# Performance work log

Measured on AMD Instinct MI355X. Metric: run time of the kernel, lower is better.

The kernel has to match this reference:

```python
import jax, jax.numpy as jnp
import numpy as np

N = 4_194_304
B = 64
H = 16
TAU = 1.0


def setup_inputs() -> dict:
    key = jax.random.key(0)
    ks = jax.random.split(key, 8)
    pos = jax.random.normal(ks[0], (N, 3), dtype=jnp.float32)
    reflectance = jax.random.uniform(ks[1], (N,), dtype=jnp.float32)
    batch = jnp.sort(jax.random.randint(ks[2], (N,), 0, B).astype(jnp.int32))
    gumbels = jax.random.gumbel(ks[3], (B, 2), dtype=jnp.float32)
    W1 = jax.random.normal(ks[4], (4, H), dtype=jnp.float32) * 0.5
    b1 = jnp.zeros((H,), dtype=jnp.float32)
    W2 = jax.random.normal(ks[5], (H, H), dtype=jnp.float32) * 0.25
    b2 = jnp.zeros((H,), dtype=jnp.float32)
    Wg = jax.random.normal(ks[6], (H, 2), dtype=jnp.float32) * 0.25
    bg = jnp.array([0.0, 2.0], dtype=jnp.float32)  # gate_nn bias init per module
    return {"pos": pos, "reflectance": reflectance, "batch": batch, "gumbels": gumbels,
            "W1": W1, "b1": b1, "W2": W2, "b2": b2, "Wg": Wg, "bg": bg}


def reference(pos, reflectance, batch, gumbels, W1, b1, W2, b2, Wg, bg):
    # point-wise MLP: [N,4] -> [N,H]
    features = jnp.concatenate([pos, reflectance[:, None]], axis=-1)
    h = jax.nn.relu(features @ W1 + b1)
    h = jax.nn.relu(h @ W2 + b2)
    # batch-indexed max pool: [N,H] -> [B,H]
    sample_features = jax.ops.segment_max(h, batch, num_segments=B)
    gate_logits = sample_features @ Wg + bg  # [B,2]
    # gumbel-softmax (hard=False as in forward)
    gate_decision = jax.nn.softmax((gate_logits + gumbels) / TAU, axis=-1)
    # gather per-point gate and scale reflectance
    use_reflectance = gate_decision[:, 1][batch]  # [N]
    return use_reflectance * reflectance
```

## Files before the change

kernel.cpp:

```cpp
#include <hip/hip_runtime.h>
#include <hip/hip_bf16.h>


#define N_PTS 4194304
#define NB 64
#define NH 16
#define WPB 4
#define SITERS 4
#define PTW (256 * SITERS)
#define PPB (WPB * PTW)
#define NBLK (N_PTS / PPB)
#define NENT (NBLK * 2)

typedef __attribute__((ext_vector_type(8))) short bf16x8;
typedef __attribute__((ext_vector_type(4))) float f32x4;
union U8 { bf16x8 v; unsigned u[4]; unsigned short s[8]; };

struct Rec { int idA, idB, bpos; };

__device__ __forceinline__ unsigned pk2(float a, float b) {
    float2 t; t.x = a; t.y = b;
    __hip_bfloat162 r = __float22bfloat162_rn(t);
    unsigned u;
    __builtin_memcpy(&u, &r, sizeof(u));
    return u;
}
__device__ __forceinline__ unsigned short f2bf(float x) {
    unsigned u = __float_as_uint(x);
    u = u + 0x7fffu + ((u >> 16) & 1u);
    return (unsigned short)(u >> 16);
}

template<bool SLOW>
__device__ __forceinline__ void do_chunk(
    const float4& q0, const float4& q1, const float4& q2, const float4& rr,
    int sb, int g, int col, int bposw,
    const U8& A1, const U8& A2, const f32x4& c1, const f32x4& c2,
    f32x4& accA, f32x4& accB)
{
    const float f[4][4] = {{q0.x, q0.y, q0.z, rr.x},
                           {q0.w, q1.x, q1.y, rr.y},
                           {q1.z, q1.w, q2.x, rr.z},
                           {q2.y, q2.z, q2.w, rr.w}};
#pragma unroll
    for (int j = 0; j < 4; ++j) {
        const unsigned F01 = pk2(f[j][0], f[j][1]);
        const unsigned F23 = pk2(f[j][2], f[j][3]);
        f32x4 d[4], h[4];
#pragma unroll
        for (int t = 0; t < 4; ++t) {
            const bool mine = (g == t);
            U8 B;
            B.u[0] = mine ? F01 : 0u;
            B.u[1] = mine ? F23 : 0u;
            B.u[2] = 0u; B.u[3] = 0u;
            d[t] = __builtin_amdgcn_mfma_f32_16x16x32_bf16(A1.v, B.v, c1, 0, 0, 0);
        }
#pragma unroll
        for (int t = 0; t < 4; ++t) {
            U8 P;
            P.u[0] = pk2(fmaxf(d[t][0], 0.f), fmaxf(d[t][1], 0.f));
            P.u[1] = pk2(fmaxf(d[t][2], 0.f), fmaxf(d[t][3], 0.f));
            P.u[2] = 0u; P.u[3] = 0u;
            h[t] = __builtin_amdgcn_mfma_f32_16x16x32_bf16(A2.v, P.v, c2, 0, 0, 0);
        }
#pragma unroll
        for (int t = 0; t < 4; ++t) {
            if (!SLOW) {
#pragma unroll
                for (int r = 0; r < 4; ++r) accA[r] = fmaxf(accA[r], h[t][r]);
            } else {
                const bool m = (sb + 4 * (16 * t + col) + j) < bposw;
#pragma unroll
                for (int r = 0; r < 4; ++r) {
                    accA[r] = fmaxf(accA[r], m ? h[t][r] : 0.f);
                    accB[r] = fmaxf(accB[r], m ? 0.f : h[t][r]);
                }
            }
        }
    }
}

__global__ __launch_bounds__(256, 4) void mlp_segmax_kernel(
    const float* __restrict__ pos,
    const float* __restrict__ refl,
    const int*   __restrict__ batch,
    const float* __restrict__ W1, const float* __restrict__ b1,
    const float* __restrict__ W2, const float* __restrict__ b2,
    float* __restrict__ pv,
    int*   __restrict__ pid,
    Rec*   __restrict__ recs)
{
    __shared__ float wlds[352];
    __shared__ float lv[WPB][2][NH];
    __shared__ int   li[WPB][2];
    __shared__ int   lbp[WPB];

    const int tid  = threadIdx.x;
    const int lane = tid & 63;
    const int wid  = tid >> 6;
    const int col  = lane & 15;
    const int g    = lane >> 4;
    const int wb   = (blockIdx.x * WPB + wid) * PTW;

    if (tid < 64)  wlds[tid]        = W1[tid];
    if (tid < 16)  wlds[64 + tid]   = b1[tid];
    wlds[80 + tid] = W2[tid];
    if (tid < 16)  wlds[336 + tid]  = b2[tid];
    __syncthreads();

    U8 A1, A2;
#pragma unroll
    for (int e = 0; e < 4; ++e) {
        A1.s[e]     = f2bf(wlds[e * NH + col]);
        A1.s[e + 4] = 0;
        A2.s[e]     = f2bf(wlds[80 + (4 * g + e) * NH + col]);
        A2.s[e + 4] = 0;
    }
    f32x4 c1, c2;
#pragma unroll
    for (int r = 0; r < 4; ++r) {
        c1[r] = wlds[64 + 4 * g + r];
        c2[r] = wlds[336 + 4 * g + r];
    }

    const int idA = batch[wb];
    const int idB = batch[wb + PTW - 1];
    const bool isSlow = (idA != idB);

    f32x4 accA = {0.f, 0.f, 0.f, 0.f};
    f32x4 accB = {0.f, 0.f, 0.f, 0.f};

    const float4* gp = (const float4*)(pos + (size_t)wb * 3);
    const float4* gr = (const float4*)(refl + wb);

    float4 q0 = gp[3 * lane + 0];
    float4 q1 = gp[3 * lane + 1];
    float4 q2 = gp[3 * lane + 2];
    float4 rr = gr[lane];

    if (!isSlow) {
#pragma unroll
        for (int s = 0; s < SITERS; ++s) {
            float4 n0, n1, n2, nr;
            if (s + 1 < SITERS) {
                n0 = gp[(s + 1) * 192 + 3 * lane + 0];
                n1 = gp[(s + 1) * 192 + 3 * lane + 1];
                n2 = gp[(s + 1) * 192 + 3 * lane + 2];
                nr = gr[(s + 1) * 64 + lane];
            }
            do_chunk<false>(q0, q1, q2, rr, wb + s * 256, g, col, 0,
                            A1, A2, c1, c2, accA, accB);
            if (s + 1 < SITERS) { q0 = n0; q1 = n1; q2 = n2; rr = nr; }
        }
    } else {
        int bposw = 0x7fffffff;
        for (int it = 0; it < PTW / 64; ++it) {
            const int idx = wb + it * 64 + lane;
            const unsigned long long mk = __ballot(batch[idx] != idA);
            if (mk) bposw = min(bposw, wb + it * 64 + (__ffsll((long long)mk) - 1));
        }
#pragma unroll
        for (int s = 0; s < SITERS; ++s) {
            float4 n0, n1, n2, nr;
            if (s + 1 < SITERS) {
                n0 = gp[(s + 1) * 192 + 3 * lane + 0];
                n1 = gp[(s + 1) * 192 + 3 * lane + 1];
                n2 = gp[(s + 1) * 192 + 3 * lane + 2];
                nr = gr[(s + 1) * 64 + lane];
            }
            do_chunk<true>(q0, q1, q2, rr, wb + s * 256, g, col, bposw,
                           A1, A2, c1, c2, accA, accB);
            if (s + 1 < SITERS) { q0 = n0; q1 = n1; q2 = n2; rr = nr; }
        }
        lbp[wid] = bposw;
    }

#pragma unroll
    for (int mk = 1; mk <= 8; mk <<= 1) {
#pragma unroll
        for (int r = 0; r < 4; ++r) {
            accA[r] = fmaxf(accA[r], __shfl_xor(accA[r], mk));
            accB[r] = fmaxf(accB[r], __shfl_xor(accB[r], mk));
        }
    }
    if (col == 0) {
        *reinterpret_cast<float4*>(&lv[wid][0][4 * g]) =
            make_float4(accA[0], accA[1], accA[2], accA[3]);
        *reinterpret_cast<float4*>(&lv[wid][1][4 * g]) =
            make_float4(accB[0], accB[1], accB[2], accB[3]);
    }
    if (lane == 0) {
        li[wid][0] = idA; li[wid][1] = idB;
        if (!isSlow) lbp[wid] = 0x7fffffff;
    }
    __syncthreads();

    if (tid < NH) {
        const int d   = tid;
        const int ida = li[0][0];
        const int idb = li[WPB - 1][1];
        float mA = 0.f, mB = 0.f;
#pragma unroll
        for (int s = 0; s < WPB; ++s)
#pragma unroll
            for (int hh = 0; hh < 2; ++hh) {
                const float val = lv[s][hh][d];
                if (li[s][hh] == ida) mA = fmaxf(mA, val);
                else                  mB = fmaxf(mB, val);
            }
        pv[(blockIdx.x * 2 + 0) * NH + d] = mA;
        pv[(blockIdx.x * 2 + 1) * NH + d] = mB;
        if (d == 0) {
            pid[blockIdx.x * 2 + 0] = ida;
            pid[blockIdx.x * 2 + 1] = idb;
            int bp = 0x7fffffff;
#pragma unroll
            for (int s = 0; s < WPB; ++s) {
                if (li[s][0] != ida) bp = min(bp, (int)(blockIdx.x * PPB + s * PTW));
                else if (lbp[s] != 0x7fffffff) bp = min(bp, lbp[s]);
            }
            Rec r; r.idA = ida; r.idB = idb; r.bpos = bp;
            recs[blockIdx.x] = r;
        }
    }
}

__global__ __launch_bounds__(256) void gate_scale_kernel(
    const float* __restrict__ refl,
    const float* __restrict__ pv,
    const int*   __restrict__ pid,
    const Rec*   __restrict__ recs,
    const float* __restrict__ Wg, const float* __restrict__ bg,
    const float* __restrict__ gum,
    float* __restrict__ out)
{
    __shared__ unsigned smA[NH], smB[NH];
    __shared__ unsigned short list[128];
    __shared__ unsigned cnt;
    __shared__ float gAB[2];

    const int tid = threadIdx.x;
    const Rec rec = recs[blockIdx.x >> 2];

    if (tid < NH) { smA[tid] = 0u; smB[tid] = 0u; }
    if (tid == 0) cnt = 0u;
    __syncthreads();

#pragma unroll
    for (int k = 0; k < NENT / 256; ++k) {
        const int e = k * 256 + tid;
        const int p = pid[e];
        const bool a = (p == rec.idA);
        const bool b = (p == rec.idB) && !a;
        if (a || b) {
            const unsigned i = atomicAdd(&cnt, 1u);
            if (i < 128u) list[i] = (unsigned short)(e | (a ? 0 : 0x8000));
        }
    }
    __syncthreads();

    const int n = (int)(cnt < 128u ? cnt : 128u);
    for (int k = tid; k < n * NH; k += 256) {
        const int i = k >> 4, d = k & 15;
        const int e = list[i] & 0x7fff;
        unsigned* dst = (list[i] & 0x8000) ? smB : smA;
        atomicMax(dst + d, __float_as_uint(pv[e * NH + d]));
    }
    __syncthreads();

    if (tid < 2) {
        const int bsel = tid ? rec.idB : rec.idA;
        const unsigned* sm = tid ? smB : smA;
        float l0 = bg[0] + gum[bsel * 2 + 0];
        float l1 = bg[1] + gum[bsel * 2 + 1];
#pragma unroll
        for (int k = 0; k < NH; ++k) {
            const float s = __uint_as_float(sm[k]);
            l0 = fmaf(s, Wg[k * 2 + 0], l0);
            l1 = fmaf(s, Wg[k * 2 + 1], l1);
        }
        gAB[tid] = 1.f / (1.f + expf(-(l1 - l0)));
    }
    __syncthreads();

    const float gA = gAB[0];
    const float gB = (rec.idA == rec.idB) ? gAB[0] : gAB[1];

    const int p0 = (blockIdx.x * 256 + tid) * 4;
    const float4 rv = *reinterpret_cast<const float4*>(refl + p0);
    float4 o;
    o.x = ((p0 + 0) < rec.bpos ? gA : gB) * rv.x;
    o.y = ((p0 + 1) < rec.bpos ? gA : gB) * rv.y;
    o.z = ((p0 + 2) < rec.bpos ? gA : gB) * rv.z;
    o.w = ((p0 + 3) < rec.bpos ? gA : gB) * rv.w;
    *reinterpret_cast<float4*>(out + p0) = o;
}

extern "C" void kernel_launch(void* const* d_in, const int* in_sizes, int n_in,
                              void* d_out, int out_size, void* d_ws, size_t ws_size,
                              hipStream_t stream) {
    const float* pos   = (const float*)d_in[0];
    const float* refl  = (const float*)d_in[1];
    const int*   batch = (const int*)d_in[2];
    const float* gumb  = (const float*)d_in[3];
    const float* W1    = (const float*)d_in[4];
    const float* b1    = (const float*)d_in[5];
    const float* W2    = (const float*)d_in[6];
    const float* b2    = (const float*)d_in[7];
    const float* Wg    = (const float*)d_in[8];
    const float* bg    = (const float*)d_in[9];
    float* out = (float*)d_out;

    float* pv   = (float*)d_ws;
    int*   pid  = (int*)((char*)d_ws + 131072);
    Rec*   recs = (Rec*)((char*)d_ws + 139264);

    mlp_segmax_kernel<<<NBLK, 256, 0, stream>>>(pos, refl, batch,
                                                W1, b1, W2, b2, pv, pid, recs);
    gate_scale_kernel<<<N_PTS / 1024, 256, 0, stream>>>(refl, pv, pid, recs,
                                                        Wg, bg, gumb, out);
}
```

Baseline: 38.98 us.

## Reduce segment max with global atomics instead of per-block partial scan

Each MLP block now atomically maxes its two per-segment partials directly into a zeroed [B,H] global table, instead of writing per-block partials and ids. The gate kernel no longer scans all block entries into shared-memory lists; it just reads the final segment maxima. This removes a full scan of the partial array from every gate block. In exchange it adds a memset launch and global atomic contention on a small table. Uint atomicMax on float bits is valid here because the post-ReLU values are non-negative.

```diff
diff --git a/kernel.cpp b/kernel.cpp
--- a/kernel.cpp
+++ b/kernel.cpp
@@ -10,7 +10,6 @@
 #define PTW (256 * SITERS)
 #define PPB (WPB * PTW)
 #define NBLK (N_PTS / PPB)
-#define NENT (NBLK * 2)
 
 typedef __attribute__((ext_vector_type(8))) short bf16x8;
 typedef __attribute__((ext_vector_type(4))) float f32x4;
@@ -87,9 +86,8 @@
     const int*   __restrict__ batch,
     const float* __restrict__ W1, const float* __restrict__ b1,
     const float* __restrict__ W2, const float* __restrict__ b2,
-    float* __restrict__ pv,
-    int*   __restrict__ pid,
-    Rec*   __restrict__ recs)
+    unsigned*    __restrict__ segmax,
+    Rec*         __restrict__ recs)
 {
     __shared__ float wlds[352];
     __shared__ float lv[WPB][2][NH];
@@ -209,11 +207,10 @@
                 if (li[s][hh] == ida) mA = fmaxf(mA, val);
                 else                  mB = fmaxf(mB, val);
             }
-        pv[(blockIdx.x * 2 + 0) * NH + d] = mA;
-        pv[(blockIdx.x * 2 + 1) * NH + d] = mB;
+        atomicMax(segmax + ida * NH + d, __float_as_uint(mA));
+        if (idb != ida)
+            atomicMax(segmax + idb * NH + d, __float_as_uint(mB));
         if (d == 0) {
-            pid[blockIdx.x * 2 + 0] = ida;
-            pid[blockIdx.x * 2 + 1] = idb;
             int bp = 0x7fffffff;
 #pragma unroll
             for (int s = 0; s < WPB; ++s) {
@@ -228,55 +225,24 @@
 
 __global__ __launch_bounds__(256) void gate_scale_kernel(
     const float* __restrict__ refl,
-    const float* __restrict__ pv,
-    const int*   __restrict__ pid,
+    const unsigned* __restrict__ segmax,
     const Rec*   __restrict__ recs,
     const float* __restrict__ Wg, const float* __restrict__ bg,
     const float* __restrict__ gum,
     float* __restrict__ out)
 {
-    __shared__ unsigned smA[NH], smB[NH];
-    __shared__ unsigned short list[128];
-    __shared__ unsigned cnt;
     __shared__ float gAB[2];
 
     const int tid = threadIdx.x;
     const Rec rec = recs[blockIdx.x >> 2];
 
-    if (tid < NH) { smA[tid] = 0u; smB[tid] = 0u; }
-    if (tid == 0) cnt = 0u;
-    __syncthreads();
-
-#pragma unroll
-    for (int k = 0; k < NENT / 256; ++k) {
-        const int e = k * 256 + tid;
-        const int p = pid[e];
-        const bool a = (p == rec.idA);
-        const bool b = (p == rec.idB) && !a;
-        if (a || b) {
-            const unsigned i = atomicAdd(&cnt, 1u);
-            if (i < 128u) list[i] = (unsigned short)(e | (a ? 0 : 0x8000));
-        }
-    }
-    __syncthreads();
-
-    const int n = (int)(cnt < 128u ? cnt : 128u);
-    for (int k = tid; k < n * NH; k += 256) {
-        const int i = k >> 4, d = k & 15;
-        const int e = list[i] & 0x7fff;
-        unsigned* dst = (list[i] & 0x8000) ? smB : smA;
-        atomicMax(dst + d, __float_as_uint(pv[e * NH + d]));
-    }
-    __syncthreads();
-
     if (tid < 2) {
         const int bsel = tid ? rec.idB : rec.idA;
-        const unsigned* sm = tid ? smB : smA;
         float l0 = bg[0] + gum[bsel * 2 + 0];
         float l1 = bg[1] + gum[bsel * 2 + 1];
 #pragma unroll
         for (int k = 0; k < NH; ++k) {
-            const float s = __uint_as_float(sm[k]);
+            const float s = __uint_as_float(segmax[bsel * NH + k]);
             l0 = fmaf(s, Wg[k * 2 + 0], l0);
             l1 = fmaf(s, Wg[k * 2 + 1], l1);
         }
@@ -312,12 +278,12 @@
     const float* bg    = (const float*)d_in[9];
     float* out = (float*)d_out;
 
-    float* pv   = (float*)d_ws;
-    int*   pid  = (int*)((char*)d_ws + 131072);
-    Rec*   recs = (Rec*)((char*)d_ws + 139264);
-
+    unsigned* segmax = (unsigned*)d_ws;
+    Rec*      recs   = (Rec*)((char*)d_ws + 4096);
+
+    (void)hipMemsetAsync(segmax, 0, NB * NH * sizeof(unsigned), stream);
     mlp_segmax_kernel<<<NBLK, 256, 0, stream>>>(pos, refl, batch,
-                                                W1, b1, W2, b2, pv, pid, recs);
-    gate_scale_kernel<<<N_PTS / 1024, 256, 0, stream>>>(refl, pv, pid, recs,
+                                                W1, b1, W2, b2, segmax, recs);
+    gate_scale_kernel<<<N_PTS / 1024, 256, 0, stream>>>(refl, segmax, recs,
                                                         Wg, bg, gumb, out);
 }
```

New measurement: 39.61 us. No clear change (+1.6%).
